# Kernel optimization log

Measured on AMD Instinct MI355X. Metric: run time of the kernel, lower is better.

The kernel has to match this reference:

```python
import jax, jax.numpy as jnp
import numpy as np
from math import sqrt

THRESHOLD = 0.5
NEG_POS_RATIO = 3
ALPHA = 1.0


def make_priors():
    fms = [(38, 0.1, [1.0, 2.0, 0.5]), (19, 0.2, [1.0, 2.0, 0.5, 3.0, 1.0 / 3]),
           (10, 0.375, [1.0, 2.0, 0.5, 3.0, 1.0 / 3]), (5, 0.55, [1.0, 2.0, 0.5, 3.0, 1.0 / 3]),
           (3, 0.725, [1.0, 2.0, 0.5]), (1, 0.9, [1.0, 2.0, 0.5])]
    scales = [0.1, 0.2, 0.375, 0.55, 0.725, 0.9]
    priors = []
    for k, (d, s, ratios) in enumerate(fms):
        for i in range(d):
            for j in range(d):
                cx = (i + 0.5) / d
                cy = (j + 0.5) / d
                for r in ratios:
                    priors.append([cx, cy, s * sqrt(r), s / sqrt(r)])
                    if r == 1.0:
                        add = sqrt(scales[k] * scales[k + 1]) if k + 1 < len(scales) else 1.0
                        priors.append([cx, cy, add, add])
    return np.clip(np.asarray(priors, dtype=np.float32), 0.0, 1.0)  # [8732, 4]


def cxcy_to_xy(b):
    return jnp.concatenate([b[..., :2] - b[..., 2:] / 2.0, b[..., :2] + b[..., 2:] / 2.0], -1)


def jaccard(a, b):
    # a: [O,4] cxcy, b: [P,4] cxcy -> IoU [O,P]
    a_xy, b_xy = cxcy_to_xy(a), cxcy_to_xy(b)
    lt = jnp.maximum(a_xy[:, None, :2], b_xy[None, :, :2])
    rb = jnp.minimum(a_xy[:, None, 2:], b_xy[None, :, 2:])
    wh = jnp.clip(rb - lt, 0.0)
    inter = wh[..., 0] * wh[..., 1]
    area_a = (a_xy[:, 2] - a_xy[:, 0]) * (a_xy[:, 3] - a_xy[:, 1])
    area_b = (b_xy[:, 2] - b_xy[:, 0]) * (b_xy[:, 3] - b_xy[:, 1])
    return inter / (area_a[:, None] + area_b[None, :] - inter)


def cxcy_to_gcxgcy(cxcy, priors):
    g_cxcy = (cxcy[..., :2] - priors[..., :2]) / (priors[..., 2:] / 10.0)
    g_wh = jnp.log(cxcy[..., 2:] / priors[..., 2:]) * 5.0
    return jnp.concatenate([g_cxcy, g_wh], -1)


def match_one(boxes_i, priors):
    # boxes_i: [O,4] cxcy
    n_obj = boxes_i.shape[0]
    ov = jaccard(boxes_i, priors)                      # [O, P]
    ov_per_prior = ov.max(0)                           # [P]
    obj_per_prior = ov.argmax(0)                       # [P]
    prior_per_obj = ov.argmax(1)                       # [O]
    obj_per_prior = obj_per_prior.at[prior_per_obj].set(jnp.arange(n_obj))
    ov_per_prior = ov_per_prior.at[prior_per_obj].set(1.0)
    labels = (ov_per_prior >= THRESHOLD).astype(jnp.int32)  # [P], 1=text 0=bg
    true_locs = cxcy_to_gcxgcy(boxes_i[obj_per_prior], priors)  # [P,4]
    return labels, true_locs


def setup_inputs() -> dict:
    key = jax.random.key(0)
    k1, k2, k3, k4 = jax.random.split(key, 4)
    priors = jnp.asarray(make_priors())
    B, P, O = 512, priors.shape[0], 16
    predicted_locs = jax.random.normal(k1, (B, P, 4), dtype=jnp.float32)
    predicted_scores = jax.random.normal(k2, (B, P, 2), dtype=jnp.float32)
    centers = 0.2 + 0.6 * jax.random.uniform(k3, (B, O, 2), dtype=jnp.float32)
    wh = 0.05 + 0.35 * jax.random.uniform(k4, (B, O, 2), dtype=jnp.float32)
    boxes = jnp.concatenate([centers, wh], -1)  # cxcy format
    return {"predicted_locs": predicted_locs, "predicted_scores": predicted_scores,
            "boxes": boxes, "priors": priors}


def reference(predicted_locs, predicted_scores, boxes, priors):
    B, P, _ = predicted_locs.shape
    labels, true_locs = jax.vmap(match_one, in_axes=(0, None))(boxes, priors)  # [B,P], [B,P,4]
    pos = labels != 0
    mask = pos.astype(predicted_locs.dtype)            # [B,P]
    n_pos = pos.sum(1)                                 # [B]

    # localization L1 loss (mean over positive box coordinates)
    loc_abs = jnp.abs(predicted_locs - true_locs).sum(-1)  # [B,P]
    loc_loss = (loc_abs * mask).sum() / (mask.sum() * 4.0)

    # per-prior cross-entropy
    logp = jax.nn.log_softmax(predicted_scores, -1)
    ce = -jnp.take_along_axis(logp, labels[..., None], -1)[..., 0]  # [B,P]

    conf_pos = (ce * mask).sum()
    ce_neg = jnp.where(pos, 0.0, ce)
    ce_neg = jnp.sort(ce_neg, axis=1)[:, ::-1]         # descending
    hard = jnp.arange(P)[None, :] < (NEG_POS_RATIO * n_pos)[:, None]
    conf_hn = (ce_neg * hard.astype(ce_neg.dtype)).sum()
    conf_loss = (conf_pos + conf_hn) / n_pos.sum().astype(predicted_locs.dtype)
    return conf_loss + ALPHA * loc_loss
```

## Files before the change

### kernel.cpp

```cpp
#include <hip/hip_runtime.h>

#define NP 8732
#define NQ (NP / 4)
#define NPT 35
#define NO 16
#define BLK 256
#define NWAVE (BLK / 64)
#define SPLIT 4
#define CHUNK (NP / SPLIT)
#define NITER ((CHUNK + BLK - 1) / BLK)


__device__ __forceinline__ float rfl(float x) {
    return __uint_as_float(__builtin_amdgcn_readfirstlane(__float_as_uint(x)));
}

__global__ __launch_bounds__(BLK, 4) void match_kernel(
    const float* __restrict__ boxes,
    const float* __restrict__ priors,
    unsigned char* __restrict__ g_obj,
    float* __restrict__ g_bv,
    int*   __restrict__ g_bi)
{
    const int b    = blockIdx.x;
    const int s    = blockIdx.y;
    const int tid  = threadIdx.x;
    const int lane = tid & 63;
    const int wv   = tid >> 6;
    const int lo = s * CHUNK, hi = lo + CHUNK;

    __shared__ float s_pv[NWAVE][NO][16];
    __shared__ int   s_pi[NWAVE][NO][16];

    float sx0[NO], sy0[NO], sx1[NO], sy1[NO], ra[NO];
    {
        const float4* bx4 = (const float4*)(boxes + (size_t)b * NO * 4);
#pragma unroll
        for (int j = 0; j < NO; j++) {
            float4 o = bx4[j];
            float hx = o.z * 0.5f, hy = o.w * 0.5f;
            sx0[j] = rfl(o.x - hx); sy0[j] = rfl(o.y - hy);
            sx1[j] = rfl(o.x + hx); sy1[j] = rfl(o.y + hy);
            ra[j]  = o.z * o.w;
        }
    }

    float tbv[NO]; int tbp[NO];
#pragma unroll
    for (int j = 0; j < NO; j++) { tbv[j] = -1.0f; tbp[j] = lo; }

    unsigned char* obj_row = g_obj + (size_t)b * NP;
    for (int k = 0; k < NITER; k++) {
        int p0 = lo + tid + k * BLK;
        bool valid = p0 < hi;
        int p = valid ? p0 : hi - 1;
        float4 pr = ((const float4*)priors)[p];
        float px0 = pr.x - pr.z * 0.5f, py0 = pr.y - pr.w * 0.5f;
        float px1 = pr.x + pr.z * 0.5f, py1 = pr.y + pr.w * 0.5f;
        float areab = pr.z * pr.w;
        if (!valid) px0 = 4.0f;
        float bv = -1.0f; int bo = 0;
#pragma unroll
        for (int j = 0; j < NO; j++) {
            bool ov = (sx1[j] >= px0) && (px1 >= sx0[j]) &&
                      (sy1[j] >= py0) && (py1 >= sy0[j]);
            if (ov) {
                float ix0 = fmaxf(sx0[j], px0);
                float iy0 = fmaxf(sy0[j], py0);
                float ix1 = fminf(sx1[j], px1);
                float iy1 = fminf(sy1[j], py1);
                float iw = fmaxf(ix1 - ix0, 0.0f);
                float ih = fmaxf(iy1 - iy0, 0.0f);
                float inter = iw * ih;
                float den = ra[j] + areab - inter;
                float iou = inter * __builtin_amdgcn_rcpf(den);
                if (iou > bv)     { bv = iou; bo = j; }
                if (iou > tbv[j]) { tbv[j] = iou; tbp[j] = p; }
            }
        }
        if (valid) obj_row[p] = (unsigned char)(bo | ((bv >= 0.5f) ? 0x80 : 0));
    }

#pragma unroll
    for (int j = 0; j < NO; j++) {
        float v = tbv[j]; int i = tbp[j];
        float v2 = __shfl_down(v, 32, 64); int i2 = __shfl_down(i, 32, 64);
        if (v2 > v || (v2 == v && i2 < i)) { v = v2; i = i2; }
        v2 = __shfl_down(v, 16, 64); i2 = __shfl_down(i, 16, 64);
        if (v2 > v || (v2 == v && i2 < i)) { v = v2; i = i2; }
        if (lane < 16) { s_pv[wv][j][lane] = v; s_pi[wv][j][lane] = i; }
    }
    __syncthreads();
    {
        const int j = tid >> 4, e = tid & 15;
        float v = s_pv[0][j][e]; int i = s_pi[0][j][e];
#pragma unroll
        for (int w = 1; w < NWAVE; w++) {
            float v2 = s_pv[w][j][e]; int i2 = s_pi[w][j][e];
            if (v2 > v || (v2 == v && i2 < i)) { v = v2; i = i2; }
        }
#pragma unroll
        for (int off = 8; off >= 1; off >>= 1) {
            float v2 = __shfl_down(v, off, 16); int i2 = __shfl_down(i, off, 16);
            if (v2 > v || (v2 == v && i2 < i)) { v = v2; i = i2; }
        }
        if (e == 0) {
            g_bv[((size_t)b * NO + j) * SPLIT + s] = v;
            g_bi[((size_t)b * NO + j) * SPLIT + s] = i;
        }
    }
}

__device__ __forceinline__ int hist_select(unsigned* hist, unsigned* s_part,
                                           unsigned* s_csuf, unsigned* s_sel,
                                           unsigned& kk, int tid, int lane, int wv)
{
    unsigned ps = 0;
#pragma unroll
    for (int i = 0; i < 16; i++) ps += hist[tid * 16 + i];
    s_part[tid] = ps;
    __syncthreads();
    if (wv == 0) {
        unsigned c0 = s_part[4 * lane + 0], c1 = s_part[4 * lane + 1];
        unsigned c2 = s_part[4 * lane + 2], c3 = s_part[4 * lane + 3];
        unsigned g = c0 + c1 + c2 + c3;
        unsigned incl = g;
#pragma unroll
        for (int off = 1; off < 64; off <<= 1) {
            unsigned o = __shfl_down(incl, off, 64);
            if (lane + off < 64) incl += o;
        }
        unsigned excl = incl - g;
        s_csuf[4 * lane + 3] = excl;
        s_csuf[4 * lane + 2] = excl + c3;
        s_csuf[4 * lane + 1] = excl + c3 + c2;
        s_csuf[4 * lane + 0] = excl + c3 + c2 + c1;
    }
    __syncthreads();
    unsigned base = s_csuf[tid];
    if (base < kk && kk <= base + s_part[tid]) {
        unsigned run = base;
        for (int i = 15; i >= 0; i--) {
            unsigned h = hist[tid * 16 + i];
            if (kk <= run + h) { s_sel[0] = (unsigned)(tid * 16 + i); s_sel[1] = kk - run; break; }
            run += h;
        }
    }
    __syncthreads();
    kk = s_sel[1];
    return (int)s_sel[0];
}

__global__ __launch_bounds__(BLK, 2) void loss_kernel(
    const float* __restrict__ plocs,
    const float* __restrict__ pscores,
    const float* __restrict__ boxes,
    const float* __restrict__ priors,
    const unsigned char* __restrict__ g_obj,
    const float* __restrict__ g_bv,
    const int*   __restrict__ g_bi,
    float* __restrict__ loc_out,
    float* __restrict__ conf_out,
    int*   __restrict__ npos_out)
{
    const int b    = blockIdx.x;
    const int tid  = threadIdx.x;
    const int lane = tid & 63;
    const int wv   = tid >> 6;

    __shared__ unsigned char s_obj[NP];
    __shared__ unsigned s_hist[4096];
    __shared__ unsigned s_part[256];
    __shared__ unsigned s_csuf[256];
    __shared__ unsigned s_sel[2];
    __shared__ float s_bcw[NO][4];
    __shared__ int   s_bestp[NO];
    __shared__ float s_tval;
    __shared__ float s_fred[3 * NWAVE];
    __shared__ int   s_ired[NWAVE];

    const unsigned* objw = (const unsigned*)(g_obj + (size_t)b * NP);
    for (int i = tid; i < NP / 4; i += BLK) ((unsigned*)s_obj)[i] = objw[i];
    if (tid < NO * 4) ((float*)s_bcw)[tid] = boxes[(size_t)b * NO * 4 + tid];
    if (tid < NO) {
        const float* bv = g_bv + ((size_t)b * NO + tid) * SPLIT;
        const int*   bi = g_bi + ((size_t)b * NO + tid) * SPLIT;
        float v = bv[0]; int i = bi[0];
#pragma unroll
        for (int s = 1; s < SPLIT; s++) {
            float v2 = bv[s]; int i2 = bi[s];
            if (v2 > v || (v2 == v && i2 < i)) { v = v2; i = i2; }
        }
        s_bestp[tid] = i;
    }
    __syncthreads();
    if (tid == 0) {
#pragma unroll
        for (int o = 0; o < NO; o++) s_obj[s_bestp[o]] = (unsigned char)(0x80 | o);
    }
    __syncthreads();

    float ce[NPT];
    float loc_sum = 0.0f, conf_pos = 0.0f; int np = 0;
    const float2* sc2 = (const float2*)(pscores + (size_t)b * NP * 2);
    const float4* pl4 = (const float4*)(plocs  + (size_t)b * NP * 4);
#pragma unroll
    for (int k = 0; k < NPT; k++) {
        int p = tid + k * BLK;
        float v = 0.0f;
        if (p < NP) {
            unsigned m = s_obj[p];
            bool pos = (m & 0x80) != 0;
            float2 s = sc2[p];
            float mx = fmaxf(s.x, s.y);
            float dd = fabsf(s.x - s.y);
            float cev = mx + __logf(1.0f + __expf(-dd)) - (pos ? s.y : s.x);
            if (pos) {
                np++;
                conf_pos += cev;
                int o = m & 15;
                float4 pr = ((const float4*)priors)[p];
                float gx = (s_bcw[o][0] - pr.x) / (pr.z / 10.0f);
                float gy = (s_bcw[o][1] - pr.y) / (pr.w / 10.0f);
                float gw = __logf(s_bcw[o][2] / pr.z) * 5.0f;
                float gh = __logf(s_bcw[o][3] / pr.w) * 5.0f;
                float4 pl = pl4[p];
                loc_sum += fabsf(pl.x - gx) + fabsf(pl.y - gy)
                         + fabsf(pl.z - gw) + fabsf(pl.w - gh);
            } else {
                v = cev;
            }
        }
        ce[k] = v;
    }

    int npw = np;
    for (int off = 32; off; off >>= 1) npw += __shfl_down(npw, off, 64);
    if (lane == 0) s_ired[wv] = npw;
    __syncthreads();
    int n_pos = 0;
#pragma unroll
    for (int w = 0; w < NWAVE; w++) n_pos += s_ired[w];

    const int K = 3 * n_pos;
    const bool selAll = (K >= NP);
    float t = 0.0f;
    if (!selAll) {
        unsigned kk = (unsigned)K;
        for (int i = tid; i < 4096; i += BLK) s_hist[i] = 0u;
        __syncthreads();
#pragma unroll
        for (int k = 0; k < NPT; k++)
            atomicAdd(&s_hist[__float_as_uint(ce[k]) >> 19], 1u);
        __syncthreads();
        unsigned b1 = (unsigned)hist_select(s_hist, s_part, s_csuf, s_sel, kk, tid, lane, wv);
        unsigned cnt1 = s_hist[b1];
        if (cnt1 == 1u) {
#pragma unroll
            for (int k = 0; k < NPT; k++)
                if ((__float_as_uint(ce[k]) >> 19) == b1) s_tval = ce[k];
            __syncthreads();
            t = s_tval;
        } else {
            __syncthreads();
            for (int i = tid; i < 4096; i += BLK) s_hist[i] = 0u;
            __syncthreads();
#pragma unroll
            for (int k = 0; k < NPT; k++) {
                unsigned u = __float_as_uint(ce[k]);
                if ((u >> 19) == b1) atomicAdd(&s_hist[(u >> 7) & 0xFFFu], 1u);
            }
            __syncthreads();
            unsigned b2 = (unsigned)hist_select(s_hist, s_part, s_csuf, s_sel, kk, tid, lane, wv);
            unsigned p2 = (b1 << 12) | b2;
            unsigned cnt2 = s_hist[b2];
            if (cnt2 == 1u) {
#pragma unroll
                for (int k = 0; k < NPT; k++)
                    if ((__float_as_uint(ce[k]) >> 7) == p2) s_tval = ce[k];
                __syncthreads();
                t = s_tval;
            } else {
                __syncthreads();
                for (int i = tid; i < 4096; i += BLK) s_hist[i] = 0u;
                __syncthreads();
#pragma unroll
                for (int k = 0; k < NPT; k++) {
                    unsigned u = __float_as_uint(ce[k]);
                    if ((u >> 7) == p2) atomicAdd(&s_hist[u & 0x7Fu], 1u);
                }
                __syncthreads();
                unsigned b3 = (unsigned)hist_select(s_hist, s_part, s_csuf, s_sel, kk, tid, lane, wv);
                t = __uint_as_float((p2 << 7) | b3);
            }
        }
    }

    float sgt = 0.0f; int cgt = 0;
#pragma unroll
    for (int k = 0; k < NPT; k++) {
        float v = ce[k];
        if (selAll || v > t) { sgt += v; cgt++; }
    }

    float a = sgt, c = conf_pos, l = loc_sum; int g = cgt;
    for (int off = 32; off; off >>= 1) {
        a += __shfl_down(a, off, 64);
        c += __shfl_down(c, off, 64);
        l += __shfl_down(l, off, 64);
        g += __shfl_down(g, off, 64);
    }
    __syncthreads();
    if (lane == 0) {
        s_fred[wv] = a; s_fred[NWAVE + wv] = c; s_fred[2 * NWAVE + wv] = l;
        s_ired[wv] = g;
    }
    __syncthreads();
    if (tid == 0) {
        float sa = 0.0f, sc = 0.0f, sl = 0.0f; int sg = 0;
#pragma unroll
        for (int w = 0; w < NWAVE; w++) {
            sa += s_fred[w]; sc += s_fred[NWAVE + w]; sl += s_fred[2 * NWAVE + w];
            sg += s_ired[w];
        }
        float conf_hn = selAll ? sa : (sa + (float)(K - sg) * t);
        conf_out[b] = sc + conf_hn;
        loc_out[b]  = sl;
        npos_out[b] = n_pos;
    }
}

__global__ __launch_bounds__(BLK, 2) void mbox_row_kernel(
    const float* __restrict__ plocs, const float* __restrict__ pscores,
    const float* __restrict__ boxes, const float* __restrict__ priors,
    float* __restrict__ loc_out, float* __restrict__ conf_out,
    int* __restrict__ npos_out)
{
    const int b = blockIdx.x, tid = threadIdx.x, lane = tid & 63, wv = tid >> 6;
    const int par = tid & 1, objLo = par << 3;
    __shared__ __align__(16) float s_ce[NP];
    __shared__ unsigned char s_obj[NP];
    __shared__ float s_bcw[NO][4], s_bxy[NO][4], s_barea[NO];
    __shared__ float s_redv[NO * NWAVE]; __shared__ int s_redi[NO * NWAVE];
    __shared__ int s_bestp[NO];
    __shared__ unsigned s_hist16[16];
    __shared__ float s_tval;
    __shared__ float s_fred[3 * NWAVE]; __shared__ int s_ired[NWAVE];

    if (tid < NO * 4) ((float*)s_bcw)[tid] = boxes[(size_t)b * NO * 4 + tid];
    __syncthreads();
    if (tid < NO) {
        float cx = s_bcw[tid][0], cy = s_bcw[tid][1], w = s_bcw[tid][2], h = s_bcw[tid][3];
        s_bxy[tid][0] = cx - w * 0.5f; s_bxy[tid][1] = cy - h * 0.5f;
        s_bxy[tid][2] = cx + w * 0.5f; s_bxy[tid][3] = cy + h * 0.5f;
        s_barea[tid] = w * h;
    }
    __syncthreads();
    float rx0[8], ry0[8], rx1[8], ry1[8], ra[8];
#pragma unroll
    for (int j = 0; j < 8; j++) {
        rx0[j] = s_bxy[objLo + j][0]; ry0[j] = s_bxy[objLo + j][1];
        rx1[j] = s_bxy[objLo + j][2]; ry1[j] = s_bxy[objLo + j][3];
        ra[j]  = s_barea[objLo + j];
    }
    float tbv[8]; int tbp[8];
#pragma unroll
    for (int j = 0; j < 8; j++) { tbv[j] = -1.0f; tbp[j] = 0; }
    for (int p = (tid >> 1); p < NP; p += (BLK / 2)) {
        float4 pr = ((const float4*)priors)[p];
        float px0 = pr.x - pr.z * 0.5f, py0 = pr.y - pr.w * 0.5f;
        float px1 = pr.x + pr.z * 0.5f, py1 = pr.y + pr.w * 0.5f;
        float areab = pr.z * pr.w;
        float bv = -1.0f; int bo = objLo;
#pragma unroll
        for (int j = 0; j < 8; j++) {
            float ix0 = fmaxf(rx0[j], px0), iy0 = fmaxf(ry0[j], py0);
            float ix1 = fminf(rx1[j], px1), iy1 = fminf(ry1[j], py1);
            float iw = fmaxf(ix1 - ix0, 0.0f), ih = fmaxf(iy1 - iy0, 0.0f);
            float inter = iw * ih, den = ra[j] + areab - inter;
            float iou = inter * __builtin_amdgcn_rcpf(den);
            if (iou > bv) { bv = iou; bo = objLo + j; }
            if (iou > tbv[j]) { tbv[j] = iou; tbp[j] = p; }
        }
        float vN = __shfl_xor(bv, 1, 64); int oN = __shfl_xor(bo, 1, 64);
        bool take = par ? (vN >= bv) : (vN > bv);
        if (take) { bv = vN; bo = oN; }
        if (par == 0) s_obj[p] = (unsigned char)(bo | ((bv >= 0.5f) ? 0x80 : 0));
    }
#pragma unroll
    for (int j = 0; j < 8; j++) {
        float v = tbv[j]; int i = tbp[j];
        for (int off = 32; off >= 2; off >>= 1) {
            float v2 = __shfl_down(v, off, 64); int i2 = __shfl_down(i, off, 64);
            if (v2 > v || (v2 == v && i2 < i)) { v = v2; i = i2; }
        }
        if (lane < 2) { s_redv[(objLo + j) * NWAVE + wv] = v; s_redi[(objLo + j) * NWAVE + wv] = i; }
    }
    __syncthreads();
    if (tid < NO) {
        float v = s_redv[tid * NWAVE]; int i = s_redi[tid * NWAVE];
#pragma unroll
        for (int w = 1; w < NWAVE; w++) {
            float v2 = s_redv[tid * NWAVE + w]; int i2 = s_redi[tid * NWAVE + w];
            if (v2 > v || (v2 == v && i2 < i)) { v = v2; i = i2; }
        }
        s_bestp[tid] = i;
    }
    __syncthreads();
    if (tid == 0) {
#pragma unroll
        for (int o = 0; o < NO; o++) s_obj[s_bestp[o]] = (unsigned char)(0x80 | o);
    }
    __syncthreads();
    float loc_sum = 0.0f, conf_pos = 0.0f; int np = 0;
    const float2* sc2 = (const float2*)(pscores + (size_t)b * NP * 2);
    const float4* pl4 = (const float4*)(plocs + (size_t)b * NP * 4);
    for (int p = tid; p < NP; p += BLK) {
        unsigned m = s_obj[p]; bool pos = (m & 0x80) != 0;
        float2 s = sc2[p];
        float mx = fmaxf(s.x, s.y), dd = fabsf(s.x - s.y);
        float cev = mx + __logf(1.0f + __expf(-dd)) - (pos ? s.y : s.x);
        if (pos) {
            np++; conf_pos += cev;
            int o = m & 15;
            float4 pr = ((const float4*)priors)[p];
            float gx = (s_bcw[o][0] - pr.x) / (pr.z / 10.0f);
            float gy = (s_bcw[o][1] - pr.y) / (pr.w / 10.0f);
            float gw = __logf(s_bcw[o][2] / pr.z) * 5.0f;
            float gh = __logf(s_bcw[o][3] / pr.w) * 5.0f;
            float4 pl = pl4[p];
            loc_sum += fabsf(pl.x - gx) + fabsf(pl.y - gy) + fabsf(pl.z - gw) + fabsf(pl.w - gh);
            s_ce[p] = 0.0f;
        } else s_ce[p] = cev;
    }
    int npw = np;
    for (int off = 32; off; off >>= 1) npw += __shfl_down(npw, off, 64);
    if (lane == 0) s_ired[wv] = npw;
    __syncthreads();
    int n_pos = 0;
#pragma unroll
    for (int w = 0; w < NWAVE; w++) n_pos += s_ired[w];
    const int K = 3 * n_pos; const bool selAll = (K >= NP);
    float t = 0.0f;
    const float4* ce4 = (const float4*)s_ce;
    if (!selAll) {
        unsigned prefix = 0u, kk = (unsigned)K; bool done = false;
        for (int shift = 28; shift >= 0 && !done; shift -= 4) {
            __syncthreads();
            if (tid < 16) s_hist16[tid] = 0u;
            __syncthreads();
            unsigned maskhi = (shift == 28) ? 0u : (0xFFFFFFFFu << (shift + 4));
            for (int q = tid; q < NQ; q += BLK) {
                float4 v = ce4[q];
#pragma unroll
                for (int j = 0; j < 4; j++) {
                    unsigned u = __float_as_uint(j == 0 ? v.x : j == 1 ? v.y : j == 2 ? v.z : v.w);
                    if ((u & maskhi) == prefix) atomicAdd(&s_hist16[(u >> shift) & 15u], 1u);
                }
            }
            __syncthreads();
            int dsel = 15; unsigned cnt;
            for (;; dsel--) { cnt = s_hist16[dsel]; if (kk <= cnt || dsel == 0) break; kk -= cnt; }
            prefix |= ((unsigned)dsel << shift);
            if (shift > 0 && cnt == 1u) {
                unsigned mh = 0xFFFFFFFFu << shift;
                for (int q = tid; q < NQ; q += BLK) {
                    float4 v = ce4[q];
#pragma unroll
                    for (int j = 0; j < 4; j++) {
                        float f = (j == 0 ? v.x : j == 1 ? v.y : j == 2 ? v.z : v.w);
                        if ((__float_as_uint(f) & mh) == prefix) s_tval = f;
                    }
                }
                __syncthreads();
                t = s_tval; done = true;
            } else if (shift == 0) t = __uint_as_float(prefix);
        }
    }
    float sgt = 0.0f; int cgt = 0;
    for (int q = tid; q < NQ; q += BLK) {
        float4 v = ce4[q];
        if (selAll || v.x > t) { sgt += v.x; cgt++; }
        if (selAll || v.y > t) { sgt += v.y; cgt++; }
        if (selAll || v.z > t) { sgt += v.z; cgt++; }
        if (selAll || v.w > t) { sgt += v.w; cgt++; }
    }
    float a = sgt, c = conf_pos, l = loc_sum; int g = cgt;
    for (int off = 32; off; off >>= 1) {
        a += __shfl_down(a, off, 64); c += __shfl_down(c, off, 64);
        l += __shfl_down(l, off, 64); g += __shfl_down(g, off, 64);
    }
    __syncthreads();
    if (lane == 0) { s_fred[wv] = a; s_fred[NWAVE + wv] = c; s_fred[2 * NWAVE + wv] = l; s_ired[wv] = g; }
    __syncthreads();
    if (tid == 0) {
        float sa = 0, sc = 0, sl = 0; int sg = 0;
#pragma unroll
        for (int w = 0; w < NWAVE; w++) { sa += s_fred[w]; sc += s_fred[NWAVE + w]; sl += s_fred[2 * NWAVE + w]; sg += s_ired[w]; }
        float conf_hn = selAll ? sa : (sa + (float)(K - sg) * t);
        conf_out[b] = sc + conf_hn; loc_out[b] = sl; npos_out[b] = n_pos;
    }
}

__global__ __launch_bounds__(256) void mbox_finalize_kernel(
    const float* __restrict__ loc_in, const float* __restrict__ conf_in,
    const int* __restrict__ npos_in, int B, float* __restrict__ out)
{
    __shared__ float sl[4], sc[4];
    __shared__ int si[4];
    int tid = threadIdx.x, lane = tid & 63, wv = tid >> 6;
    float l = 0.0f, c = 0.0f; int n = 0;
    for (int i = tid; i < B; i += 256) { l += loc_in[i]; c += conf_in[i]; n += npos_in[i]; }
    for (int off = 32; off; off >>= 1) {
        l += __shfl_down(l, off, 64);
        c += __shfl_down(c, off, 64);
        n += __shfl_down(n, off, 64);
    }
    if (lane == 0) { sl[wv] = l; sc[wv] = c; si[wv] = n; }
    __syncthreads();
    if (tid == 0) {
        float tl = sl[0] + sl[1] + sl[2] + sl[3];
        float tc = sc[0] + sc[1] + sc[2] + sc[3];
        int tn = si[0] + si[1] + si[2] + si[3];
        float fn = (float)tn;
        out[0] = tc / fn + tl / (fn * 4.0f);
    }
}

extern "C" void kernel_launch(void* const* d_in, const int* in_sizes, int n_in,
                              void* d_out, int out_size, void* d_ws, size_t ws_size,
                              hipStream_t stream) {
    const float* plocs   = (const float*)d_in[0];
    const float* pscores = (const float*)d_in[1];
    const float* boxes   = (const float*)d_in[2];
    const float* priors  = (const float*)d_in[3];
    const int B = in_sizes[0] / (NP * 4);

    float* loc_ws  = (float*)d_ws;
    float* conf_ws = loc_ws + B;
    int*   np_ws   = (int*)(conf_ws + B);
    float* g_bv    = (float*)(np_ws + B);
    int*   g_bi    = (int*)(g_bv + (size_t)B * NO * SPLIT);
    unsigned char* g_obj = (unsigned char*)(g_bi + (size_t)B * NO * SPLIT);
    size_t need = (size_t)(3 * B) * 4 + (size_t)B * NO * SPLIT * 8 + (size_t)B * NP;

    if (ws_size >= need) {
        match_kernel<<<dim3(B, SPLIT), BLK, 0, stream>>>(boxes, priors, g_obj, g_bv, g_bi);
        loss_kernel<<<B, BLK, 0, stream>>>(plocs, pscores, boxes, priors,
                                           g_obj, g_bv, g_bi, loc_ws, conf_ws, np_ws);
    } else {
        mbox_row_kernel<<<B, BLK, 0, stream>>>(plocs, pscores, boxes, priors,
                                               loc_ws, conf_ws, np_ws);
    }
    mbox_finalize_kernel<<<1, 256, 0, stream>>>(loc_ws, conf_ws, np_ws, B, (float*)d_out);
}
```

Before: 194.6 us.

## Split loss into per-chunk CE kernel and per-row select kernel; branchless IoU

The per-row loss kernel becomes two kernels. A ce_kernel spreads each row over SPLIT blocks to compute cross-entropy, positive counts and the localization sum, and writes the per-prior negative CE to a global buffer. A select_kernel then reads that buffer with float4 loads and runs the histogram top-K selection. This gives more parallelism for the memory-bound CE stage, at the cost of an extra B×NP float round-trip through global memory and one more kernel launch. The IoU loop in match_kernel also drops its overlap-test branch and computes every box unconditionally to avoid divergence.

Measured after the change: 244.3 us. 25.5% more time.

```diff
diff --git a/kernel.cpp b/kernel.cpp
--- a/kernel.cpp
+++ b/kernel.cpp
@@ -3,6 +3,7 @@
 #define NP 8732
 #define NQ (NP / 4)
 #define NPT 35
+#define NSEL 36
 #define NO 16
 #define BLK 256
 #define NWAVE (BLK / 64)
@@ -62,21 +63,17 @@
         float bv = -1.0f; int bo = 0;
 #pragma unroll
         for (int j = 0; j < NO; j++) {
-            bool ov = (sx1[j] >= px0) && (px1 >= sx0[j]) &&
-                      (sy1[j] >= py0) && (py1 >= sy0[j]);
-            if (ov) {
-                float ix0 = fmaxf(sx0[j], px0);
-                float iy0 = fmaxf(sy0[j], py0);
-                float ix1 = fminf(sx1[j], px1);
-                float iy1 = fminf(sy1[j], py1);
-                float iw = fmaxf(ix1 - ix0, 0.0f);
-                float ih = fmaxf(iy1 - iy0, 0.0f);
-                float inter = iw * ih;
-                float den = ra[j] + areab - inter;
-                float iou = inter * __builtin_amdgcn_rcpf(den);
-                if (iou > bv)     { bv = iou; bo = j; }
-                if (iou > tbv[j]) { tbv[j] = iou; tbp[j] = p; }
-            }
+            float ix0 = fmaxf(sx0[j], px0);
+            float iy0 = fmaxf(sy0[j], py0);
+            float ix1 = fminf(sx1[j], px1);
+            float iy1 = fminf(sy1[j], py1);
+            float iw = fmaxf(ix1 - ix0, 0.0f);
+            float ih = fmaxf(iy1 - iy0, 0.0f);
+            float inter = iw * ih;
+            float den = ra[j] + areab - inter;
+            float iou = inter * __builtin_amdgcn_rcpf(den);
+            if (iou > bv)     { bv = iou; bo = j; }
+            if (iou > tbv[j]) { tbv[j] = iou; tbp[j] = p; }
         }
         if (valid) obj_row[p] = (unsigned char)(bo | ((bv >= 0.5f) ? 0x80 : 0));
     }
@@ -111,6 +108,104 @@
     }
 }
 
+__global__ __launch_bounds__(BLK, 8) void ce_kernel(
+    const float* __restrict__ plocs,
+    const float* __restrict__ pscores,
+    const float* __restrict__ boxes,
+    const float* __restrict__ priors,
+    const unsigned char* __restrict__ g_obj,
+    const float* __restrict__ g_bv,
+    const int*   __restrict__ g_bi,
+    float* __restrict__ ce_g,
+    float* __restrict__ loc_c,
+    float* __restrict__ conf_c,
+    int*   __restrict__ np_c)
+{
+    const int b    = blockIdx.x;
+    const int s    = blockIdx.y;
+    const int tid  = threadIdx.x;
+    const int lane = tid & 63;
+    const int wv   = tid >> 6;
+    const int lo = s * CHUNK, hi = lo + CHUNK;
+
+    __shared__ unsigned char s_objc[CHUNK];
+    __shared__ float s_bcw[NO][4];
+    __shared__ int   s_bestp[NO];
+    __shared__ float s_fred[2 * NWAVE];
+    __shared__ int   s_ired[NWAVE];
+
+    const unsigned char* orow = g_obj + (size_t)b * NP + lo;
+    for (int i = tid; i < CHUNK; i += BLK) s_objc[i] = orow[i];
+    if (tid < NO * 4) ((float*)s_bcw)[tid] = boxes[(size_t)b * NO * 4 + tid];
+    if (tid < NO) {
+        const float* bv = g_bv + ((size_t)b * NO + tid) * SPLIT;
+        const int*   bi = g_bi + ((size_t)b * NO + tid) * SPLIT;
+        float v = bv[0]; int i = bi[0];
+#pragma unroll
+        for (int t = 1; t < SPLIT; t++) {
+            float v2 = bv[t]; int i2 = bi[t];
+            if (v2 > v || (v2 == v && i2 < i)) { v = v2; i = i2; }
+        }
+        s_bestp[tid] = i;
+    }
+    __syncthreads();
+    if (tid == 0) {
+#pragma unroll
+        for (int o = 0; o < NO; o++) {
+            int p = s_bestp[o];
+            if (p >= lo && p < hi) s_objc[p - lo] = (unsigned char)(0x80 | o);
+        }
+    }
+    __syncthreads();
+
+    float loc_sum = 0.0f, conf_pos = 0.0f; int np = 0;
+    const float2* sc2 = (const float2*)(pscores + (size_t)b * NP * 2);
+    const float4* pl4 = (const float4*)(plocs  + (size_t)b * NP * 4);
+    float* cerow = ce_g + (size_t)b * NP;
+    for (int p = lo + tid; p < hi; p += BLK) {
+        unsigned m = s_objc[p - lo];
+        bool pos = (m & 0x80) != 0;
+        float2 sc = sc2[p];
+        float mx = fmaxf(sc.x, sc.y);
+        float dd = fabsf(sc.x - sc.y);
+        float cev = mx + __logf(1.0f + __expf(-dd)) - (pos ? sc.y : sc.x);
+        float v = 0.0f;
+        if (pos) {
+            np++;
+            conf_pos += cev;
+            int o = m & 15;
+            float4 pr = ((const float4*)priors)[p];
+            float gx = (s_bcw[o][0] - pr.x) / (pr.z / 10.0f);
+            float gy = (s_bcw[o][1] - pr.y) / (pr.w / 10.0f);
+            float gw = __logf(s_bcw[o][2] / pr.z) * 5.0f;
+            float gh = __logf(s_bcw[o][3] / pr.w) * 5.0f;
+            float4 pl = pl4[p];
+            loc_sum += fabsf(pl.x - gx) + fabsf(pl.y - gy)
+                     + fabsf(pl.z - gw) + fabsf(pl.w - gh);
+        } else {
+            v = cev;
+        }
+        cerow[p] = v;
+    }
+
+    int npw = np; float cw = conf_pos, lw = loc_sum;
+    for (int off = 32; off; off >>= 1) {
+        npw += __shfl_down(npw, off, 64);
+        cw  += __shfl_down(cw, off, 64);
+        lw  += __shfl_down(lw, off, 64);
+    }
+    if (lane == 0) { s_ired[wv] = npw; s_fred[wv] = cw; s_fred[NWAVE + wv] = lw; }
+    __syncthreads();
+    if (tid == 0) {
+        int n = 0; float c = 0.0f, l = 0.0f;
+#pragma unroll
+        for (int w = 0; w < NWAVE; w++) { n += s_ired[w]; c += s_fred[w]; l += s_fred[NWAVE + w]; }
+        np_c[b * SPLIT + s]   = n;
+        conf_c[b * SPLIT + s] = c;
+        loc_c[b * SPLIT + s]  = l;
+    }
+}
+
 __device__ __forceinline__ int hist_select(unsigned* hist, unsigned* s_part,
                                            unsigned* s_csuf, unsigned* s_sel,
                                            unsigned& kk, int tid, int lane, int wv)
@@ -151,96 +246,39 @@
     return (int)s_sel[0];
 }
 
-__global__ __launch_bounds__(BLK, 2) void loss_kernel(
-    const float* __restrict__ plocs,
-    const float* __restrict__ pscores,
-    const float* __restrict__ boxes,
-    const float* __restrict__ priors,
-    const unsigned char* __restrict__ g_obj,
-    const float* __restrict__ g_bv,
-    const int*   __restrict__ g_bi,
-    float* __restrict__ loc_out,
-    float* __restrict__ conf_out,
-    int*   __restrict__ npos_out)
+__global__ __launch_bounds__(BLK, 2) void select_kernel(
+    const float* __restrict__ ce_g,
+    const int*   __restrict__ np_c,
+    float* __restrict__ chn_out)
 {
     const int b    = blockIdx.x;
     const int tid  = threadIdx.x;
     const int lane = tid & 63;
     const int wv   = tid >> 6;
 
-    __shared__ unsigned char s_obj[NP];
     __shared__ unsigned s_hist[4096];
     __shared__ unsigned s_part[256];
     __shared__ unsigned s_csuf[256];
     __shared__ unsigned s_sel[2];
-    __shared__ float s_bcw[NO][4];
-    __shared__ int   s_bestp[NO];
     __shared__ float s_tval;
-    __shared__ float s_fred[3 * NWAVE];
+    __shared__ float s_fred[NWAVE];
     __shared__ int   s_ired[NWAVE];
 
-    const unsigned* objw = (const unsigned*)(g_obj + (size_t)b * NP);
-    for (int i = tid; i < NP / 4; i += BLK) ((unsigned*)s_obj)[i] = objw[i];
-    if (tid < NO * 4) ((float*)s_bcw)[tid] = boxes[(size_t)b * NO * 4 + tid];
-    if (tid < NO) {
-        const float* bv = g_bv + ((size_t)b * NO + tid) * SPLIT;
-        const int*   bi = g_bi + ((size_t)b * NO + tid) * SPLIT;
-        float v = bv[0]; int i = bi[0];
-#pragma unroll
-        for (int s = 1; s < SPLIT; s++) {
-            float v2 = bv[s]; int i2 = bi[s];
-            if (v2 > v || (v2 == v && i2 < i)) { v = v2; i = i2; }
-        }
-        s_bestp[tid] = i;
-    }
-    __syncthreads();
-    if (tid == 0) {
-#pragma unroll
-        for (int o = 0; o < NO; o++) s_obj[s_bestp[o]] = (unsigned char)(0x80 | o);
-    }
-    __syncthreads();
-
-    float ce[NPT];
-    float loc_sum = 0.0f, conf_pos = 0.0f; int np = 0;
-    const float2* sc2 = (const float2*)(pscores + (size_t)b * NP * 2);
-    const float4* pl4 = (const float4*)(plocs  + (size_t)b * NP * 4);
-#pragma unroll
-    for (int k = 0; k < NPT; k++) {
-        int p = tid + k * BLK;
-        float v = 0.0f;
-        if (p < NP) {
-            unsigned m = s_obj[p];
-            bool pos = (m & 0x80) != 0;
-            float2 s = sc2[p];
-            float mx = fmaxf(s.x, s.y);
-            float dd = fabsf(s.x - s.y);
-            float cev = mx + __logf(1.0f + __expf(-dd)) - (pos ? s.y : s.x);
-            if (pos) {
-                np++;
-                conf_pos += cev;
-                int o = m & 15;
-                float4 pr = ((const float4*)priors)[p];
-                float gx = (s_bcw[o][0] - pr.x) / (pr.z / 10.0f);
-                float gy = (s_bcw[o][1] - pr.y) / (pr.w / 10.0f);
-                float gw = __logf(s_bcw[o][2] / pr.z) * 5.0f;
-                float gh = __logf(s_bcw[o][3] / pr.w) * 5.0f;
-                float4 pl = pl4[p];
-                loc_sum += fabsf(pl.x - gx) + fabsf(pl.y - gy)
-                         + fabsf(pl.z - gw) + fabsf(pl.w - gh);
-            } else {
-                v = cev;
-            }
-        }
-        ce[k] = v;
-    }
-
-    int npw = np;
-    for (int off = 32; off; off >>= 1) npw += __shfl_down(npw, off, 64);
-    if (lane == 0) s_ired[wv] = npw;
-    __syncthreads();
+    float ce[NSEL];
+    const float4* ce4 = (const float4*)(ce_g + (size_t)b * NP);
+#pragma unroll
+    for (int k = 0; k < 9; k++) {
+        int q = tid + k * BLK;
+        float4 v;
+        if (q < NQ) v = ce4[q];
+        else { v.x = 0.0f; v.y = 0.0f; v.z = 0.0f; v.w = 0.0f; }
+        ce[4 * k + 0] = v.x; ce[4 * k + 1] = v.y;
+        ce[4 * k + 2] = v.z; ce[4 * k + 3] = v.w;
+    }
+
     int n_pos = 0;
 #pragma unroll
-    for (int w = 0; w < NWAVE; w++) n_pos += s_ired[w];
+    for (int t = 0; t < SPLIT; t++) n_pos += np_c[b * SPLIT + t];
 
     const int K = 3 * n_pos;
     const bool selAll = (K >= NP);
@@ -250,14 +288,14 @@
         for (int i = tid; i < 4096; i += BLK) s_hist[i] = 0u;
         __syncthreads();
 #pragma unroll
-        for (int k = 0; k < NPT; k++)
+        for (int k = 0; k < NSEL; k++)
             atomicAdd(&s_hist[__float_as_uint(ce[k]) >> 19], 1u);
         __syncthreads();
         unsigned b1 = (unsigned)hist_select(s_hist, s_part, s_csuf, s_sel, kk, tid, lane, wv);
         unsigned cnt1 = s_hist[b1];
         if (cnt1 == 1u) {
 #pragma unroll
-            for (int k = 0; k < NPT; k++)
+            for (int k = 0; k < NSEL; k++)
                 if ((__float_as_uint(ce[k]) >> 19) == b1) s_tval = ce[k];
             __syncthreads();
             t = s_tval;
@@ -266,7 +304,7 @@
             for (int i = tid; i < 4096; i += BLK) s_hist[i] = 0u;
             __syncthreads();
 #pragma unroll
-            for (int k = 0; k < NPT; k++) {
+            for (int k = 0; k < NSEL; k++) {
                 unsigned u = __float_as_uint(ce[k]);
                 if ((u >> 19) == b1) atomicAdd(&s_hist[(u >> 7) & 0xFFFu], 1u);
             }
@@ -276,7 +314,7 @@
             unsigned cnt2 = s_hist[b2];
             if (cnt2 == 1u) {
 #pragma unroll
-                for (int k = 0; k < NPT; k++)
+                for (int k = 0; k < NSEL; k++)
                     if ((__float_as_uint(ce[k]) >> 7) == p2) s_tval = ce[k];
                 __syncthreads();
                 t = s_tval;
@@ -285,7 +323,7 @@
                 for (int i = tid; i < 4096; i += BLK) s_hist[i] = 0u;
                 __syncthreads();
 #pragma unroll
-                for (int k = 0; k < NPT; k++) {
+                for (int k = 0; k < NSEL; k++) {
                     unsigned u = __float_as_uint(ce[k]);
                     if ((u >> 7) == p2) atomicAdd(&s_hist[u & 0x7Fu], 1u);
                 }
@@ -298,35 +336,53 @@
 
     float sgt = 0.0f; int cgt = 0;
 #pragma unroll
-    for (int k = 0; k < NPT; k++) {
+    for (int k = 0; k < NSEL; k++) {
         float v = ce[k];
         if (selAll || v > t) { sgt += v; cgt++; }
     }
 
-    float a = sgt, c = conf_pos, l = loc_sum; int g = cgt;
+    float a = sgt; int g = cgt;
     for (int off = 32; off; off >>= 1) {
         a += __shfl_down(a, off, 64);
+        g += __shfl_down(g, off, 64);
+    }
+    __syncthreads();
+    if (lane == 0) { s_fred[wv] = a; s_ired[wv] = g; }
+    __syncthreads();
+    if (tid == 0) {
+        float sa = 0.0f; int sg = 0;
+#pragma unroll
+        for (int w = 0; w < NWAVE; w++) { sa += s_fred[w]; sg += s_ired[w]; }
+        chn_out[b] = selAll ? sa : (sa + (float)(K - sg) * t);
+    }
+}
+
+__global__ __launch_bounds__(256) void mbox_finalize2_kernel(
+    const float* __restrict__ loc_c, const float* __restrict__ conf_c,
+    const int* __restrict__ np_c, const float* __restrict__ chn,
+    int B, float* __restrict__ out)
+{
+    __shared__ float sl[4], sc[4];
+    __shared__ int si[4];
+    int tid = threadIdx.x, lane = tid & 63, wv = tid >> 6;
+    float l = 0.0f, c = 0.0f; int n = 0;
+    for (int i = tid; i < B * SPLIT; i += 256) {
+        l += loc_c[i]; c += conf_c[i]; n += np_c[i];
+    }
+    for (int i = tid; i < B; i += 256) c += chn[i];
+    for (int off = 32; off; off >>= 1) {
+        l += __shfl_down(l, off, 64);
         c += __shfl_down(c, off, 64);
-        l += __shfl_down(l, off, 64);
-        g += __shfl_down(g, off, 64);
-    }
-    __syncthreads();
-    if (lane == 0) {
-        s_fred[wv] = a; s_fred[NWAVE + wv] = c; s_fred[2 * NWAVE + wv] = l;
-        s_ired[wv] = g;
-    }
+        n += __shfl_down(n, off, 64);
+    }
+    if (lane == 0) { sl[wv] = l; sc[wv] = c; si[wv] = n; }
     __syncthreads();
     if (tid == 0) {
-        float sa = 0.0f, sc = 0.0f, sl = 0.0f; int sg = 0;
-#pragma unroll
-        for (int w = 0; w < NWAVE; w++) {
-            sa += s_fred[w]; sc += s_fred[NWAVE + w]; sl += s_fred[2 * NWAVE + w];
-            sg += s_ired[w];
-        }
-        float conf_hn = selAll ? sa : (sa + (float)(K - sg) * t);
-        conf_out[b] = sc + conf_hn;
-        loc_out[b]  = sl;
-        npos_out[b] = n_pos;
+        float tl = sl[0] + sl[1] + sl[2] + sl[3];
+        float tc = sc[0] + sc[1] + sc[2] + sc[3];
+        int tn = si[0] + si[1] + si[2] + si[3];
+        float fn = (float)tn;
+        out[0] = tc / fn + tl / (fn * 4.0f);
     }
 }
 
@@ -536,21 +592,31 @@
     const float* priors  = (const float*)d_in[3];
     const int B = in_sizes[0] / (NP * 4);
 
-    float* loc_ws  = (float*)d_ws;
-    float* conf_ws = loc_ws + B;
-    int*   np_ws   = (int*)(conf_ws + B);
-    float* g_bv    = (float*)(np_ws + B);
-    int*   g_bi    = (int*)(g_bv + (size_t)B * NO * SPLIT);
-    unsigned char* g_obj = (unsigned char*)(g_bi + (size_t)B * NO * SPLIT);
-    size_t need = (size_t)(3 * B) * 4 + (size_t)B * NO * SPLIT * 8 + (size_t)B * NP;
+    float* loc_c  = (float*)d_ws;
+    float* conf_c = loc_c + (size_t)B * SPLIT;
+    int*   np_c   = (int*)(conf_c + (size_t)B * SPLIT);
+    float* chn_ws = (float*)(np_c + (size_t)B * SPLIT);
+    float* g_bv   = chn_ws + B;
+    int*   g_bi   = (int*)(g_bv + (size_t)B * NO * SPLIT);
+    float* ce_g   = (float*)(g_bi + (size_t)B * NO * SPLIT);
+    unsigned char* g_obj = (unsigned char*)(ce_g + (size_t)B * NP);
+    size_t need = (size_t)B * SPLIT * 12 + (size_t)B * 4
+                + (size_t)B * NO * SPLIT * 8 + (size_t)B * NP * 5;
 
     if (ws_size >= need) {
         match_kernel<<<dim3(B, SPLIT), BLK, 0, stream>>>(boxes, priors, g_obj, g_bv, g_bi);
-        loss_kernel<<<B, BLK, 0, stream>>>(plocs, pscores, boxes, priors,
-                                           g_obj, g_bv, g_bi, loc_ws, conf_ws, np_ws);
+        ce_kernel<<<dim3(B, SPLIT), BLK, 0, stream>>>(plocs, pscores, boxes, priors,
+                                                      g_obj, g_bv, g_bi,
+                                                      ce_g, loc_c, conf_c, np_c);
+        select_kernel<<<B, BLK, 0, stream>>>(ce_g, np_c, chn_ws);
+        mbox_finalize2_kernel<<<1, 256, 0, stream>>>(loc_c, conf_c, np_c, chn_ws,
+                                                     B, (float*)d_out);
     } else {
+        float* loc_ws  = (float*)d_ws;
+        float* conf_ws = loc_ws + B;
+        int*   np_ws   = (int*)(conf_ws + B);
         mbox_row_kernel<<<B, BLK, 0, stream>>>(plocs, pscores, boxes, priors,
                                                loc_ws, conf_ws, np_ws);
-    }
-    mbox_finalize_kernel<<<1, 256, 0, stream>>>(loc_ws, conf_ws, np_ws, B, (float*)d_out);
-}
+        mbox_finalize_kernel<<<1, 256, 0, stream>>>(loc_ws, conf_ws, np_ws, B, (float*)d_out);
+    }
+}
```
